# Optimization experiments

Hardware: AMD Instinct MI355X
Metric: run time of the kernel (lower is better)

The kernel has to match this reference:

```python
import jax, jax.numpy as jnp
import numpy as np

N_EMBD = 1024
N_HEAD = 16
HEAD_DIM = N_EMBD // N_HEAD


def setup_inputs() -> dict:
    key = jax.random.key(0)
    kx, kq, kk, kv, ko = jax.random.split(key, 5)
    B, T = 4, 2048
    x = jax.random.normal(kx, (B, T, N_EMBD), dtype=jnp.float32)
    s = N_EMBD ** -0.5
    Wq = jax.random.normal(kq, (N_EMBD, N_EMBD), dtype=jnp.float32) * s
    Wk = jax.random.normal(kk, (N_EMBD, HEAD_DIM), dtype=jnp.float32) * s
    Wv = jax.random.normal(kv, (N_EMBD, HEAD_DIM), dtype=jnp.float32) * s
    Wo = jax.random.normal(ko, (N_EMBD, N_EMBD), dtype=jnp.float32) * s
    return {"x": x, "Wq": Wq, "Wk": Wk, "Wv": Wv, "Wo": Wo}


def reference(x, Wq, Wk, Wv, Wo):
    B, T, C = x.shape
    scale = HEAD_DIM ** -0.5
    # q: [B, H, T, D]; shared k, v: [B, T, D]
    q = (x @ Wq).reshape(B, T, N_HEAD, HEAD_DIM).transpose(0, 2, 1, 3)
    k = x @ Wk
    v = x @ Wv
    # scores: [B, H, T, T] (shared K head broadcast over H)
    att = jnp.einsum('bhtd,bsd->bhts', q, k) * scale
    causal = jnp.tril(jnp.ones((T, T), dtype=bool))
    att = jnp.where(causal, att, -jnp.inf)
    att = jax.nn.softmax(att, axis=-1)
    out = jnp.einsum('bhts,bsd->bhtd', att, v)  # [B, H, T, D]
    out = out.transpose(0, 2, 1, 3).reshape(B, T, C)
    return out @ Wo
```

## Files before the change

kernel.cpp:

```cpp
#include <hip/hip_runtime.h>

typedef __attribute__((ext_vector_type(8))) short short8;
typedef __attribute__((ext_vector_type(4))) float f32x4;

__device__ __forceinline__ unsigned short f2bf(float f) {
  unsigned u = __builtin_bit_cast(unsigned, f);
  u += 0x7fffu + ((u >> 16) & 1u);
  return (unsigned short)(u >> 16);
}
__device__ __forceinline__ unsigned pack_bf2(float lo, float hi) {
  return (unsigned)f2bf(lo) | ((unsigned)f2bf(hi) << 16);
}

#define GLDS16(g, l)                                                          \
  __builtin_amdgcn_global_load_lds(                                           \
      (const __attribute__((address_space(1))) void*)(g),                     \
      (__attribute__((address_space(3))) void*)(l), 16, 0, 0)

#define QSCALE 0.18033688011112042f

__global__ void cast_x_bf16(const float4* __restrict__ in,
                            ushort4* __restrict__ out, int n4) {
  int i = blockIdx.x * blockDim.x + threadIdx.x;
  if (i >= n4) return;
  float4 v = in[i];
  ushort4 o;
  o.x = f2bf(v.x); o.y = f2bf(v.y); o.z = f2bf(v.z); o.w = f2bf(v.w);
  out[i] = o;
}

__global__ void transpose_cvt_all(const float* __restrict__ Wq,
                                  const float* __restrict__ Wk,
                                  const float* __restrict__ Wv,
                                  const float* __restrict__ Wo,
                                  unsigned short* __restrict__ Wcat,
                                  unsigned short* __restrict__ Wot) {
  __shared__ float tile[32][33];
  const int z = blockIdx.z;
  int bx = blockIdx.x;
  const float* in;
  unsigned short* out;
  int N;
  if (z == 0)      { in = Wq; out = Wcat;               N = 1024; }
  else if (z == 1) { in = Wo; out = Wot;                N = 1024; }
  else {
    if (bx < 2)      { in = Wk; out = Wcat + 1024 * 1024; N = 64; }
    else if (bx < 4) { in = Wv; out = Wcat + 1088 * 1024; N = 64; bx -= 2; }
    else return;
  }
  const int K = 1024;
  const int n0 = bx * 32, k0 = blockIdx.y * 32;
  const int tx = threadIdx.x, ty = threadIdx.y;
#pragma unroll
  for (int i = 0; i < 4; ++i)
    tile[ty + 8 * i][tx] = in[(size_t)(k0 + ty + 8 * i) * N + n0 + tx];
  __syncthreads();
#pragma unroll
  for (int i = 0; i < 4; ++i)
    out[(size_t)(n0 + ty + 8 * i) * K + k0 + tx] = f2bf(tile[tx][ty + 8 * i]);
}

template <int EPI>
__global__ __launch_bounds__(256) void gemm_bt(
    const unsigned short* __restrict__ A, const unsigned short* __restrict__ Bt,
    unsigned short* __restrict__ Cq, unsigned short* __restrict__ Ck,
    unsigned short* __restrict__ Cv, float* __restrict__ Cf, int N, int K) {
  __shared__ __align__(16) unsigned short As[128 * 64];
  __shared__ __align__(16) unsigned short Bs[128 * 64];
  const int tid = threadIdx.x;
  const int w = tid >> 6, lane = tid & 63;
  const int nwg = gridDim.x * gridDim.y;
  const int lid = blockIdx.y * gridDim.x + blockIdx.x;
  const int cpx = nwg >> 3;
  const int swz = (lid & 7) * cpx + (lid >> 3);
  const int m0 = (swz / gridDim.x) * 128, n0 = (swz % gridDim.x) * 128;
  const int wm = (w >> 1) * 64, wn = (w & 1) * 64;
  const int g = lane >> 4, c = lane & 15;
  const int lr = lane >> 3, lc = (lane & 7) * 8;

  f32x4 acc[4][4] = {};

  for (int k0 = 0; k0 < K; k0 += 64) {
#pragma unroll
    for (int i = 0; i < 4; ++i) {
      int ci = w * 4 + i;
      GLDS16(A + (size_t)(m0 + ci * 8 + lr) * K + k0 + lc, As + ci * 512);
      GLDS16(Bt + (size_t)(n0 + ci * 8 + lr) * K + k0 + lc, Bs + ci * 512);
    }
    __syncthreads();
#pragma unroll
    for (int kk = 0; kk < 2; ++kk) {
      const int col = kk * 32 + g * 8;
      short8 av[4], bv[4];
#pragma unroll
      for (int mi = 0; mi < 4; ++mi)
        av[mi] = *(const short8*)(As + (wm + mi * 16 + c) * 64 + col);
#pragma unroll
      for (int ni = 0; ni < 4; ++ni)
        bv[ni] = *(const short8*)(Bs + (wn + ni * 16 + c) * 64 + col);
#pragma unroll
      for (int mi = 0; mi < 4; ++mi)
#pragma unroll
        for (int ni = 0; ni < 4; ++ni)
          acc[mi][ni] = __builtin_amdgcn_mfma_f32_16x16x32_bf16(
              av[mi], bv[ni], acc[mi][ni], 0, 0, 0);
    }
    __syncthreads();
  }

#pragma unroll
  for (int mi = 0; mi < 4; ++mi) {
#pragma unroll
    for (int ni = 0; ni < 4; ++ni) {
      f32x4 a = acc[mi][ni];
      const int col = n0 + wn + ni * 16 + c;
#pragma unroll
      for (int r = 0; r < 4; ++r) {
        const int row = m0 + wm + mi * 16 + g * 4 + r;
        float v = a[r];
        if (EPI == 0) {
          if (col < 1024)
            Cq[(size_t)row * 1024 + col] = f2bf(v * QSCALE);
          else if (col < 1088)
            Ck[(size_t)row * 64 + (col - 1024)] = f2bf(v);
          else
            Cv[((size_t)(row >> 11) * 64 + (col - 1088)) * 2048 + (row & 2047)] =
                f2bf(v);
        } else {
          Cf[(size_t)row * N + col] = v;
        }
      }
    }
  }
}

__global__ __launch_bounds__(512, 4) void attn_mqa(
    const unsigned short* __restrict__ Q, const unsigned short* __restrict__ Kb,
    const unsigned short* __restrict__ Vt, unsigned short* __restrict__ Oc) {
  __shared__ __align__(16) unsigned short Kl[2][64 * 64];
  __shared__ __align__(16) unsigned short Vl[2][64 * 64];
  __shared__ __align__(16) unsigned short Pl[8][16 * 72];
  const int tid = threadIdx.x;
  const int w = tid >> 6, lane = tid & 63;
  const int pairi = blockIdx.x;
  const int hp = blockIdx.y;
  const int b = blockIdx.z;
  const int h = hp * 2 + (w >> 2);
  const int wq = w & 3;
  const int g = lane >> 4, c = lane & 15;
  const int swr = (c & 7) * 8;
  const int srow = tid >> 3;
  const int scs = ((tid & 7) ^ (srow & 7)) * 8;
  const unsigned short* Kbase = Kb + (size_t)b * 2048 * 64;
  const unsigned short* Vbase = Vt + (size_t)b * 64 * 2048;
  unsigned short* pw = Pl[w];
  unsigned* pd = (unsigned*)pw;

  short8 ones;
#pragma unroll
  for (int j = 0; j < 8; ++j) ones[j] = (short)0x3F80;

#pragma unroll 1
  for (int half = 0; half < 2; ++half) {
    const int qt = half ? (31 - pairi) : pairi;
    const int qb = qt * 64 + wq * 16;
    const int qi = qb + c;

    short8 qf[2];
#pragma unroll
    for (int kk = 0; kk < 2; ++kk)
      qf[kk] = *(const short8*)(Q + (size_t)(b * 2048 + qb + c) * 1024 +
                                h * 64 + kk * 32 + g * 8);

    f32x4 po[4] = {};
    f32x4 lac = {};
    float m = -1e30f;

    GLDS16(Kbase + (size_t)srow * 64 + scs, &Kl[0][0] + tid * 8);
    GLDS16(Vbase + (size_t)srow * 2048 + scs, &Vl[0][0] + tid * 8);
    const unsigned short* kpf = Kbase + (size_t)(64 + srow) * 64 + scs;
    const unsigned short* vpf = Vbase + (size_t)srow * 2048 + 64 + scs;
    int cur = 0;

    for (int it = 0; it <= qt; ++it) {
      __syncthreads();

      if (it < qt) {
        GLDS16(kpf, &Kl[cur ^ 1][0] + tid * 8);
        GLDS16(vpf, &Vl[cur ^ 1][0] + tid * 8);
        kpf += 64 * 64;
        vpf += 64;
      }

      const unsigned short* Kt = &Kl[cur][0];
      const unsigned short* Vc = &Vl[cur][0];
      const int kv0 = it * 64;

      f32x4 s[4] = {};
      __builtin_amdgcn_s_setprio(1);
#pragma unroll
      for (int kk = 0; kk < 2; ++kk) {
        const int col = (kk * 32 + g * 8) ^ swr;
#pragma unroll
        for (int f = 0; f < 4; ++f) {
          short8 kf = *(const short8*)(Kt + (f * 16 + c) * 64 + col);
          s[f] = __builtin_amdgcn_mfma_f32_16x16x32_bf16(kf, qf[kk], s[f], 0, 0, 0);
        }
      }
      __builtin_amdgcn_s_setprio(0);

      if (it == qt) {
#pragma unroll
        for (int f = 0; f < 4; ++f)
#pragma unroll
          for (int r = 0; r < 4; ++r)
            if (kv0 + f * 16 + g * 4 + r > qi) s[f][r] = -1e30f;
      }

      const float t0 = fmaxf(fmaxf(s[0][0], s[0][1]), s[0][2]);
      const float t1 = fmaxf(fmaxf(s[0][3], s[1][0]), s[1][1]);
      const float t2 = fmaxf(fmaxf(s[1][2], s[1][3]), s[2][0]);
      const float t3 = fmaxf(fmaxf(s[2][1], s[2][2]), s[2][3]);
      const float t4 = fmaxf(fmaxf(s[3][0], s[3][1]), s[3][2]);
      const float u0 = fmaxf(fmaxf(t0, t1), t2);
      const float u1 = fmaxf(fmaxf(t3, t4), s[3][3]);
      float pm = fmaxf(u0, u1);

      if (!__all(pm <= m + 8.0f)) {
        pm = fmaxf(pm, __shfl_xor(pm, 16, 64));
        pm = fmaxf(pm, __shfl_xor(pm, 32, 64));
        const float mn = fmaxf(m, pm);
        const float al = __builtin_amdgcn_exp2f(m - mn);
        m = mn;
#pragma unroll
        for (int r = 0; r < 4; ++r) {
          const float ar = __shfl(al, g * 4 + r, 64);
          lac[r] *= ar;
#pragma unroll
          for (int fd = 0; fd < 4; ++fd) po[fd][r] *= ar;
        }
      }

#pragma unroll
      for (int f = 0; f < 4; ++f) {
        const float p0 = __builtin_amdgcn_exp2f(s[f][0] - m);
        const float p1 = __builtin_amdgcn_exp2f(s[f][1] - m);
        const float p2 = __builtin_amdgcn_exp2f(s[f][2] - m);
        const float p3 = __builtin_amdgcn_exp2f(s[f][3] - m);
        uint2 pk;
        pk.x = pack_bf2(p0, p1);
        pk.y = pack_bf2(p2, p3);
        *(uint2*)(pd + c * 36 + f * 8 + g * 2) = pk;
      }

      __builtin_amdgcn_s_setprio(1);
#pragma unroll
      for (int kk = 0; kk < 2; ++kk) {
        short8 pa = *(const short8*)(pw + c * 72 + kk * 32 + g * 8);
        lac = __builtin_amdgcn_mfma_f32_16x16x32_bf16(pa, ones, lac, 0, 0, 0);
        const int col = (kk * 32 + g * 8) ^ swr;
#pragma unroll
        for (int fd = 0; fd < 4; ++fd) {
          short8 vf = *(const short8*)(Vc + (fd * 16 + c) * 64 + col);
          po[fd] = __builtin_amdgcn_mfma_f32_16x16x32_bf16(pa, vf, po[fd], 0, 0, 0);
        }
      }
      __builtin_amdgcn_s_setprio(0);
      cur ^= 1;
    }

    __syncthreads();

#pragma unroll
    for (int r = 0; r < 4; ++r) {
      const float inv = __builtin_amdgcn_rcpf(lac[r]);
      const int trow = qb + g * 4 + r;
#pragma unroll
      for (int fd = 0; fd < 4; ++fd)
        Oc[(size_t)(b * 2048 + trow) * 1024 + h * 64 + fd * 16 + c] =
            f2bf(po[fd][r] * inv);
    }
  }
}

extern "C" void kernel_launch(void* const* d_in, const int* in_sizes, int n_in,
                              void* d_out, int out_size, void* d_ws,
                              size_t ws_size, hipStream_t stream) {
  const float* x = (const float*)d_in[0];
  const float* Wq = (const float*)d_in[1];
  const float* Wk = (const float*)d_in[2];
  const float* Wv = (const float*)d_in[3];
  const float* Wo = (const float*)d_in[4];
  float* out = (float*)d_out;

  char* ws = (char*)d_ws;
  unsigned short* xb   = (unsigned short*)ws;
  unsigned short* Qb   = (unsigned short*)(ws + (size_t)(16u << 20));
  unsigned short* Attn = (unsigned short*)(ws + (size_t)(32u << 20));
  unsigned short* Wcat = (unsigned short*)(ws + (size_t)(48u << 20));
  unsigned short* Wot  = (unsigned short*)(ws + (size_t)(48u << 20) + 2359296);
  unsigned short* Kb   = (unsigned short*)(ws + (size_t)(48u << 20) + 2359296 + 2097152);
  unsigned short* Vtb  = (unsigned short*)(ws + (size_t)(48u << 20) + 2359296 + 2097152 + 1048576);

  cast_x_bf16<<<8192, 256, 0, stream>>>((const float4*)x, (ushort4*)xb, 2097152);
  transpose_cvt_all<<<dim3(32, 32, 3), dim3(32, 8), 0, stream>>>(Wq, Wk, Wv, Wo,
                                                                 Wcat, Wot);

  gemm_bt<0><<<dim3(9, 64), 256, 0, stream>>>(xb, Wcat, Qb, Kb, Vtb, nullptr,
                                              1152, 1024);

  attn_mqa<<<dim3(16, 8, 4), 512, 0, stream>>>(Qb, Kb, Vtb, Attn);

  gemm_bt<1><<<dim3(8, 64), 256, 0, stream>>>(Attn, Wot, nullptr, nullptr,
                                              nullptr, out, 1024, 1024);
}
```

Baseline: 154.0 us.

## Restructure MQA attention into 1024-thread blocks with four heads and separate V transpose

The attention kernel now launches 512 blocks of 1024 threads, one query tile per block covering four heads. Each block no longer processes a pair of causal tiles; the pairing is moved into a block-index ordering instead. The K/V tile loads are split so half the threads load K and half load V. The scattered transposed V store in the QKV GEMM epilogue is replaced by a row-major store plus a separate transpose kernel. Probability packing switches from round-to-nearest to truncation via a byte permute, saving ALU at a small precision cost.

```diff
diff --git a/kernel.cpp b/kernel.cpp
--- a/kernel.cpp
+++ b/kernel.cpp
@@ -8,8 +8,9 @@
   u += 0x7fffu + ((u >> 16) & 1u);
   return (unsigned short)(u >> 16);
 }
-__device__ __forceinline__ unsigned pack_bf2(float lo, float hi) {
-  return (unsigned)f2bf(lo) | ((unsigned)f2bf(hi) << 16);
+__device__ __forceinline__ unsigned pack_bf2_rtz(float p0, float p1) {
+  return __builtin_amdgcn_perm(__builtin_bit_cast(unsigned, p1),
+                               __builtin_bit_cast(unsigned, p0), 0x07060302u);
 }
 
 #define GLDS16(g, l)                                                          \
@@ -60,6 +61,24 @@
     out[(size_t)(n0 + ty + 8 * i) * K + k0 + tx] = f2bf(tile[tx][ty + 8 * i]);
 }
 
+__global__ void transpose_v(const unsigned short* __restrict__ Vr,
+                            unsigned short* __restrict__ Vt) {
+  __shared__ unsigned short tile[32][34];
+  const int t0 = blockIdx.x * 32;
+  const int d0 = blockIdx.y * 32;
+  const int b = blockIdx.z;
+  const int tx = threadIdx.x, ty = threadIdx.y;
+#pragma unroll
+  for (int i = 0; i < 4; ++i)
+    tile[ty + 8 * i][tx] =
+        Vr[(size_t)(b * 2048 + t0 + ty + 8 * i) * 64 + d0 + tx];
+  __syncthreads();
+#pragma unroll
+  for (int i = 0; i < 4; ++i)
+    Vt[((size_t)b * 64 + d0 + ty + 8 * i) * 2048 + t0 + tx] =
+        tile[tx][ty + 8 * i];
+}
+
 template <int EPI>
 __global__ __launch_bounds__(256) void gemm_bt(
     const unsigned short* __restrict__ A, const unsigned short* __restrict__ Bt,
@@ -124,8 +143,7 @@
           else if (col < 1088)
             Ck[(size_t)row * 64 + (col - 1024)] = f2bf(v);
           else
-            Cv[((size_t)(row >> 11) * 64 + (col - 1088)) * 2048 + (row & 2047)] =
-                f2bf(v);
+            Cv[(size_t)row * 64 + (col - 1088)] = f2bf(v);
         } else {
           Cf[(size_t)row * N + col] = v;
         }
@@ -134,25 +152,34 @@
   }
 }
 
-__global__ __launch_bounds__(512, 4) void attn_mqa(
+__global__ __launch_bounds__(1024, 8) void attn_mqa(
     const unsigned short* __restrict__ Q, const unsigned short* __restrict__ Kb,
     const unsigned short* __restrict__ Vt, unsigned short* __restrict__ Oc) {
   __shared__ __align__(16) unsigned short Kl[2][64 * 64];
   __shared__ __align__(16) unsigned short Vl[2][64 * 64];
-  __shared__ __align__(16) unsigned short Pl[8][16 * 72];
+  __shared__ __align__(16) unsigned short Pl[16][16 * 72];
   const int tid = threadIdx.x;
   const int w = tid >> 6, lane = tid & 63;
-  const int pairi = blockIdx.x;
-  const int hp = blockIdx.y;
-  const int b = blockIdx.z;
-  const int h = hp * 2 + (w >> 2);
+  const int bid = blockIdx.x;
+  const int hq = (bid >> 2) & 3;
+  const int b = bid & 3;
+  const int qi16 = (bid >> 4) & 15;
+  const int qt = (bid < 256) ? qi16 : 31 - qi16;
+  const int h = hq * 4 + (w >> 2);
   const int wq = w & 3;
   const int g = lane >> 4, c = lane & 15;
   const int swr = (c & 7) * 8;
-  const int srow = tid >> 3;
-  const int scs = ((tid & 7) ^ (srow & 7)) * 8;
+  const int sh = tid >> 9;
+  const int st = tid & 511;
+  const int srow = st >> 3;
+  const int scs = ((st & 7) ^ (srow & 7)) * 8;
   const unsigned short* Kbase = Kb + (size_t)b * 2048 * 64;
   const unsigned short* Vbase = Vt + (size_t)b * 64 * 2048;
+  const unsigned short* sp = sh ? Vbase + (size_t)srow * 2048 + scs
+                                : Kbase + (size_t)srow * 64 + scs;
+  const ptrdiff_t sstep = sh ? 64 : 4096;
+  unsigned short* ld0 = (sh ? &Vl[0][0] : &Kl[0][0]) + st * 8;
+  unsigned short* ld1 = (sh ? &Vl[1][0] : &Kl[1][0]) + st * 8;
   unsigned short* pw = Pl[w];
   unsigned* pd = (unsigned*)pw;
 
@@ -160,126 +187,116 @@
 #pragma unroll
   for (int j = 0; j < 8; ++j) ones[j] = (short)0x3F80;
 
-#pragma unroll 1
-  for (int half = 0; half < 2; ++half) {
-    const int qt = half ? (31 - pairi) : pairi;
-    const int qb = qt * 64 + wq * 16;
-    const int qi = qb + c;
-
-    short8 qf[2];
-#pragma unroll
-    for (int kk = 0; kk < 2; ++kk)
-      qf[kk] = *(const short8*)(Q + (size_t)(b * 2048 + qb + c) * 1024 +
-                                h * 64 + kk * 32 + g * 8);
-
-    f32x4 po[4] = {};
-    f32x4 lac = {};
-    float m = -1e30f;
-
-    GLDS16(Kbase + (size_t)srow * 64 + scs, &Kl[0][0] + tid * 8);
-    GLDS16(Vbase + (size_t)srow * 2048 + scs, &Vl[0][0] + tid * 8);
-    const unsigned short* kpf = Kbase + (size_t)(64 + srow) * 64 + scs;
-    const unsigned short* vpf = Vbase + (size_t)srow * 2048 + 64 + scs;
-    int cur = 0;
-
-    for (int it = 0; it <= qt; ++it) {
-      __syncthreads();
-
-      if (it < qt) {
-        GLDS16(kpf, &Kl[cur ^ 1][0] + tid * 8);
-        GLDS16(vpf, &Vl[cur ^ 1][0] + tid * 8);
-        kpf += 64 * 64;
-        vpf += 64;
+  const int qb = qt * 64 + wq * 16;
+  const int qi = qb + c;
+
+  short8 qf[2];
+#pragma unroll
+  for (int kk = 0; kk < 2; ++kk)
+    qf[kk] = *(const short8*)(Q + (size_t)(b * 2048 + qb + c) * 1024 +
+                              h * 64 + kk * 32 + g * 8);
+
+  f32x4 po[4] = {};
+  f32x4 lac = {};
+  float m = -1e30f;
+
+  GLDS16(sp, ld0);
+  sp += sstep;
+  int cur = 0;
+
+  for (int it = 0; it <= qt; ++it) {
+    __syncthreads();
+
+    if (it < qt) {
+      GLDS16(sp, cur ? ld0 : ld1);
+      sp += sstep;
+    }
+
+    const unsigned short* Kt = &Kl[cur][0];
+    const unsigned short* Vc = &Vl[cur][0];
+    const int kv0 = it * 64;
+
+    f32x4 s[4] = {};
+    __builtin_amdgcn_s_setprio(1);
+#pragma unroll
+    for (int kk = 0; kk < 2; ++kk) {
+      const int col = (kk * 32 + g * 8) ^ swr;
+#pragma unroll
+      for (int f = 0; f < 4; ++f) {
+        short8 kf = *(const short8*)(Kt + (f * 16 + c) * 64 + col);
+        s[f] = __builtin_amdgcn_mfma_f32_16x16x32_bf16(kf, qf[kk], s[f], 0, 0, 0);
       }
-
-      const unsigned short* Kt = &Kl[cur][0];
-      const unsigned short* Vc = &Vl[cur][0];
-      const int kv0 = it * 64;
-
-      f32x4 s[4] = {};
-      __builtin_amdgcn_s_setprio(1);
-#pragma unroll
-      for (int kk = 0; kk < 2; ++kk) {
-        const int col = (kk * 32 + g * 8) ^ swr;
-#pragma unroll
-        for (int f = 0; f < 4; ++f) {
-          short8 kf = *(const short8*)(Kt + (f * 16 + c) * 64 + col);
-          s[f] = __builtin_amdgcn_mfma_f32_16x16x32_bf16(kf, qf[kk], s[f], 0, 0, 0);
-        }
+    }
+    __builtin_amdgcn_s_setprio(0);
+
+    if (it == qt) {
+#pragma unroll
+      for (int f = 0; f < 4; ++f)
+#pragma unroll
+        for (int r = 0; r < 4; ++r)
+          if (kv0 + f * 16 + g * 4 + r > qi) s[f][r] = -1e30f;
+    }
+
+    const float t0 = fmaxf(fmaxf(s[0][0], s[0][1]), s[0][2]);
+    const float t1 = fmaxf(fmaxf(s[0][3], s[1][0]), s[1][1]);
+    const float t2 = fmaxf(fmaxf(s[1][2], s[1][3]), s[2][0]);
+    const float t3 = fmaxf(fmaxf(s[2][1], s[2][2]), s[2][3]);
+    const float t4 = fmaxf(fmaxf(s[3][0], s[3][1]), s[3][2]);
+    const float u0 = fmaxf(fmaxf(t0, t1), t2);
+    const float u1 = fmaxf(fmaxf(t3, t4), s[3][3]);
+    float pm = fmaxf(u0, u1);
+
+    if (!__all(pm <= m + 8.0f)) {
+      pm = fmaxf(pm, __shfl_xor(pm, 16, 64));
+      pm = fmaxf(pm, __shfl_xor(pm, 32, 64));
+      const float mn = fmaxf(m, pm);
+      const float al = __builtin_amdgcn_exp2f(m - mn);
+      m = mn;
+#pragma unroll
+      for (int r = 0; r < 4; ++r) {
+        const float ar = __shfl(al, g * 4 + r, 64);
+        lac[r] *= ar;
+#pragma unroll
+        for (int fd = 0; fd < 4; ++fd) po[fd][r] *= ar;
       }
-      __builtin_amdgcn_s_setprio(0);
-
-      if (it == qt) {
-#pragma unroll
-        for (int f = 0; f < 4; ++f)
-#pragma unroll
-          for (int r = 0; r < 4; ++r)
-            if (kv0 + f * 16 + g * 4 + r > qi) s[f][r] = -1e30f;
+    }
+
+#pragma unroll
+    for (int f = 0; f < 4; ++f) {
+      const float p0 = __builtin_amdgcn_exp2f(s[f][0] - m);
+      const float p1 = __builtin_amdgcn_exp2f(s[f][1] - m);
+      const float p2 = __builtin_amdgcn_exp2f(s[f][2] - m);
+      const float p3 = __builtin_amdgcn_exp2f(s[f][3] - m);
+      uint2 pk;
+      pk.x = pack_bf2_rtz(p0, p1);
+      pk.y = pack_bf2_rtz(p2, p3);
+      *(uint2*)(pd + c * 36 + f * 8 + g * 2) = pk;
+    }
+
+    __builtin_amdgcn_s_setprio(1);
+#pragma unroll
+    for (int kk = 0; kk < 2; ++kk) {
+      short8 pa = *(const short8*)(pw + c * 72 + kk * 32 + g * 8);
+      lac = __builtin_amdgcn_mfma_f32_16x16x32_bf16(pa, ones, lac, 0, 0, 0);
+      const int col = (kk * 32 + g * 8) ^ swr;
+#pragma unroll
+      for (int fd = 0; fd < 4; ++fd) {
+        short8 vf = *(const short8*)(Vc + (fd * 16 + c) * 64 + col);
+        po[fd] = __builtin_amdgcn_mfma_f32_16x16x32_bf16(pa, vf, po[fd], 0, 0, 0);
       }
-
-      const float t0 = fmaxf(fmaxf(s[0][0], s[0][1]), s[0][2]);
-      const float t1 = fmaxf(fmaxf(s[0][3], s[1][0]), s[1][1]);
-      const float t2 = fmaxf(fmaxf(s[1][2], s[1][3]), s[2][0]);
-      const float t3 = fmaxf(fmaxf(s[2][1], s[2][2]), s[2][3]);
-      const float t4 = fmaxf(fmaxf(s[3][0], s[3][1]), s[3][2]);
-      const float u0 = fmaxf(fmaxf(t0, t1), t2);
-      const float u1 = fmaxf(fmaxf(t3, t4), s[3][3]);
-      float pm = fmaxf(u0, u1);
-
-      if (!__all(pm <= m + 8.0f)) {
-        pm = fmaxf(pm, __shfl_xor(pm, 16, 64));
-        pm = fmaxf(pm, __shfl_xor(pm, 32, 64));
-        const float mn = fmaxf(m, pm);
-        const float al = __builtin_amdgcn_exp2f(m - mn);
-        m = mn;
-#pragma unroll
-        for (int r = 0; r < 4; ++r) {
-          const float ar = __shfl(al, g * 4 + r, 64);
-          lac[r] *= ar;
-#pragma unroll
-          for (int fd = 0; fd < 4; ++fd) po[fd][r] *= ar;
-        }
-      }
-
-#pragma unroll
-      for (int f = 0; f < 4; ++f) {
-        const float p0 = __builtin_amdgcn_exp2f(s[f][0] - m);
-        const float p1 = __builtin_amdgcn_exp2f(s[f][1] - m);
-        const float p2 = __builtin_amdgcn_exp2f(s[f][2] - m);
-        const float p3 = __builtin_amdgcn_exp2f(s[f][3] - m);
-        uint2 pk;
-        pk.x = pack_bf2(p0, p1);
-        pk.y = pack_bf2(p2, p3);
-        *(uint2*)(pd + c * 36 + f * 8 + g * 2) = pk;
-      }
-
-      __builtin_amdgcn_s_setprio(1);
-#pragma unroll
-      for (int kk = 0; kk < 2; ++kk) {
-        short8 pa = *(const short8*)(pw + c * 72 + kk * 32 + g * 8);
-        lac = __builtin_amdgcn_mfma_f32_16x16x32_bf16(pa, ones, lac, 0, 0, 0);
-        const int col = (kk * 32 + g * 8) ^ swr;
-#pragma unroll
-        for (int fd = 0; fd < 4; ++fd) {
-          short8 vf = *(const short8*)(Vc + (fd * 16 + c) * 64 + col);
-          po[fd] = __builtin_amdgcn_mfma_f32_16x16x32_bf16(pa, vf, po[fd], 0, 0, 0);
-        }
-      }
-      __builtin_amdgcn_s_setprio(0);
-      cur ^= 1;
-    }
-
-    __syncthreads();
-
-#pragma unroll
-    for (int r = 0; r < 4; ++r) {
-      const float inv = __builtin_amdgcn_rcpf(lac[r]);
-      const int trow = qb + g * 4 + r;
-#pragma unroll
-      for (int fd = 0; fd < 4; ++fd)
-        Oc[(size_t)(b * 2048 + trow) * 1024 + h * 64 + fd * 16 + c] =
-            f2bf(po[fd][r] * inv);
-    }
+    }
+    __builtin_amdgcn_s_setprio(0);
+    cur ^= 1;
+  }
+
+#pragma unroll
+  for (int r = 0; r < 4; ++r) {
+    const float inv = __builtin_amdgcn_rcpf(lac[r]);
+    const int trow = qb + g * 4 + r;
+#pragma unroll
+    for (int fd = 0; fd < 4; ++fd)
+      Oc[(size_t)(b * 2048 + trow) * 1024 + h * 64 + fd * 16 + c] =
+          f2bf(po[fd][r] * inv);
   }
 }
 
@@ -301,15 +318,17 @@
   unsigned short* Wot  = (unsigned short*)(ws + (size_t)(48u << 20) + 2359296);
   unsigned short* Kb   = (unsigned short*)(ws + (size_t)(48u << 20) + 2359296 + 2097152);
   unsigned short* Vtb  = (unsigned short*)(ws + (size_t)(48u << 20) + 2359296 + 2097152 + 1048576);
+  unsigned short* Vrow = Attn;
 
   cast_x_bf16<<<8192, 256, 0, stream>>>((const float4*)x, (ushort4*)xb, 2097152);
   transpose_cvt_all<<<dim3(32, 32, 3), dim3(32, 8), 0, stream>>>(Wq, Wk, Wv, Wo,
                                                                  Wcat, Wot);
 
-  gemm_bt<0><<<dim3(9, 64), 256, 0, stream>>>(xb, Wcat, Qb, Kb, Vtb, nullptr,
+  gemm_bt<0><<<dim3(9, 64), 256, 0, stream>>>(xb, Wcat, Qb, Kb, Vrow, nullptr,
                                               1152, 1024);
-
-  attn_mqa<<<dim3(16, 8, 4), 512, 0, stream>>>(Qb, Kb, Vtb, Attn);
+  transpose_v<<<dim3(64, 2, 4), dim3(32, 8), 0, stream>>>(Vrow, Vtb);
+
+  attn_mqa<<<512, 1024, 0, stream>>>(Qb, Kb, Vtb, Attn);
 
   gemm_bt<1><<<dim3(8, 64), 256, 0, stream>>>(Attn, Wot, nullptr, nullptr,
                                               nullptr, out, 1024, 1024);
```

Result: no change. 153.8 us (-0.2%).
